# Optimization experiments

Measured on AMD Instinct MI355X. Metric: run time of the kernel, lower is better.

The kernel has to match this reference:

```python
import jax, jax.numpy as jnp
import numpy as np

N, E, IN, HID, HEADS, OUT = 20000, 320000, 64, 32, 8, 128
EPS_SM = 1e-16


def setup_inputs() -> dict:
    key = jax.random.key(0)
    ks = iter(jax.random.split(key, 40))
    def g(shape, scale=0.1):
        return jax.random.normal(next(ks), shape, dtype=jnp.float32) * scale
    inp = {
        "x": jax.random.normal(next(ks), (N, IN), dtype=jnp.float32),
        "edge_index": jax.random.randint(next(ks), (2, E), 0, N, dtype=jnp.int64),
        # layer 0: GATConv(64 -> 32, heads=8, concat) => dim 256
        "W0": g((IN, HEADS * HID)), "b0": jnp.zeros((HEADS * HID,), jnp.float32),
        "as0": g((HEADS, HID)), "ad0": g((HEADS, HID)),
        "lng0": jnp.ones((HEADS * HID,), jnp.float32), "lnb0": jnp.zeros((HEADS * HID,), jnp.float32),
        "rW0": g((IN, HEADS * HID)), "rb0": jnp.zeros((HEADS * HID,), jnp.float32),
        "rw0": jnp.ones((1,), jnp.float32),
        # layer 1: GATConv(256 -> 32, heads=8, concat) => dim 256, residual = Identity
        "W1": g((HEADS * HID, HEADS * HID)), "b1": jnp.zeros((HEADS * HID,), jnp.float32),
        "as1": g((HEADS, HID)), "ad1": g((HEADS, HID)),
        "lng1": jnp.ones((HEADS * HID,), jnp.float32), "lnb1": jnp.zeros((HEADS * HID,), jnp.float32),
        "rw1": jnp.ones((1,), jnp.float32),
        # layer 2: GATConv(256 -> 128, heads=8, concat=False mean) => dim 128
        "W2": g((HEADS * HID, HEADS * OUT)), "b2": jnp.zeros((OUT,), jnp.float32),
        "as2": g((HEADS, OUT)), "ad2": g((HEADS, OUT)),
        "lng2": jnp.ones((OUT,), jnp.float32), "lnb2": jnp.zeros((OUT,), jnp.float32),
        "rW2": g((HEADS * HID, OUT)), "rb2": jnp.zeros((OUT,), jnp.float32),
        "rw2": jnp.ones((1,), jnp.float32),
    }
    return inp


def _gat_conv(x, src, dst, W, b, a_s, a_d, heads, out_c, concat):
    n = x.shape[0]
    h = (x @ W).reshape(n, heads, out_c)            # [N,H,C]
    al_s = jnp.sum(h * a_s, axis=-1)                 # [N,H]
    al_d = jnp.sum(h * a_d, axis=-1)
    e = jax.nn.leaky_relu(al_s[src] + al_d[dst], 0.2)  # [E,H]
    m = jax.ops.segment_max(e, dst, num_segments=n)
    m = jnp.where(jnp.isfinite(m), m, 0.0)
    ex = jnp.exp(e - m[dst])
    denom = jax.ops.segment_sum(ex, dst, num_segments=n)
    alpha = ex / (denom[dst] + EPS_SM)               # [E,H]
    msg = alpha[:, :, None] * h[src]                 # [E,H,C]
    out = jax.ops.segment_sum(msg, dst, num_segments=n)  # [N,H,C]
    if concat:
        return out.reshape(n, heads * out_c) + b
    return out.mean(axis=1) + b


def _layer_norm(x, g, b, eps=1e-5):
    mu = x.mean(-1, keepdims=True)
    var = x.var(-1, keepdims=True)
    return (x - mu) * jax.lax.rsqrt(var + eps) * g + b


def reference(x, edge_index, W0, b0, as0, ad0, lng0, lnb0, rW0, rb0, rw0,
              W1, b1, as1, ad1, lng1, lnb1, rw1,
              W2, b2, as2, ad2, lng2, lnb2, rW2, rb2, rw2):
    ei = edge_index.astype(jnp.int32)
    ar = jnp.arange(N, dtype=jnp.int32)
    src = jnp.concatenate([ei[0], ar])               # add self loops
    dst = jnp.concatenate([ei[1], ar])

    # layer 0 (eval mode: dropout is identity)
    g0 = _gat_conv(x, src, dst, W0, b0, as0, ad0, HEADS, HID, True)
    h = _layer_norm(g0, lng0, lnb0) + jax.nn.sigmoid(rw0) * (x @ rW0 + rb0)
    h = jax.nn.elu(h)

    # layer 1 (residual projection = Identity)
    g1 = _gat_conv(h, src, dst, W1, b1, as1, ad1, HEADS, HID, True)
    h = jax.nn.elu(_layer_norm(g1, lng1, lnb1) + jax.nn.sigmoid(rw1) * h)

    # layer 2 (concat=False -> mean over heads)
    g2 = _gat_conv(h, src, dst, W2, b2, as2, ad2, HEADS, OUT, False)
    out = _layer_norm(g2, lng2, lnb2) + jax.nn.sigmoid(rw2) * (h @ rW2 + rb2)
    return out
```

## Files before the change

### kernel.cpp

```cpp
#include <hip/hip_runtime.h>
#include <cstddef>
#include <cstdint>

#define NN 20000
#define EE 320000
#define ET (EE + NN)
#define CH 64

typedef __attribute__((ext_vector_type(8))) short bf16x8;
typedef __attribute__((ext_vector_type(4))) float f32x4;

__device__ __forceinline__ unsigned short f2bf_rne(float f) {
  unsigned int u = __float_as_uint(f);
  u += 0x7FFF + ((u >> 16) & 1);
  return (unsigned short)(u >> 16);
}

__device__ __forceinline__ float bf2f(unsigned short b) {
  return __uint_as_float(((unsigned int)b) << 16);
}


__global__ __launch_bounds__(256) void zero_i32(int* __restrict__ p, int n) {
  int i = blockIdx.x * 256 + threadIdx.x;
  if (i < n) p[i] = 0;
}

__global__ __launch_bounds__(256) void zero_f32(float* __restrict__ p, int n) {
  int i = blockIdx.x * 256 + threadIdx.x;
  if (i < n) p[i] = 0.f;
}

__global__ __launch_bounds__(256) void cvt_bf16(const float* __restrict__ src,
                                                unsigned short* __restrict__ dst, int n) {
  int i = blockIdx.x * 256 + threadIdx.x;
  if (i < n) dst[i] = f2bf_rne(src[i]);
}

__global__ void tconv(const float* __restrict__ src, unsigned short* __restrict__ dst,
                      int N) {
  int n = blockIdx.x, k = threadIdx.x, K = blockDim.x;
  dst[(size_t)n * K + k] = f2bf_rne(src[(size_t)k * N + n]);
}

__global__ void build_v16(const float* __restrict__ W2, const float* __restrict__ as2,
                          const float* __restrict__ ad2, unsigned short* __restrict__ V16) {
  int r = blockIdx.x, k = threadIdx.x;
  int h = r & 7;
  const float* av = (r < 8) ? (as2 + h * 128) : (ad2 + h * 128);
  const float* wr = W2 + (size_t)k * 1024 + h * 128;
  float v = 0.f;
#pragma unroll 4
  for (int c = 0; c < 128; ++c) v += wr[c] * av[c];
  V16[(size_t)r * 256 + k] = f2bf_rne(v);
}

__global__ void build_wstk(const float* __restrict__ W2, unsigned short* __restrict__ WT) {
  int c = blockIdx.x, k = threadIdx.x;
#pragma unroll
  for (int h = 0; h < 8; ++h)
    WT[(size_t)c * 2048 + h * 256 + k] = f2bf_rne(0.125f * W2[(size_t)k * 1024 + h * 128 + c]);
}


__global__ __launch_bounds__(256) void count_kernel(const int* __restrict__ ei,
                                                    int* __restrict__ deg) {
  int e = blockIdx.x * 256 + threadIdx.x;
  if (e < EE) {
    int d = ei[EE + e];
    if (d >= 0 && d < NN) atomicAdd(&deg[d], 1);
  }
}

__global__ __launch_bounds__(1024) void scan_blk(const int* __restrict__ deg,
    int* __restrict__ offs, int* __restrict__ bsum) {
  __shared__ int s[1024];
  int b = blockIdx.x, tid = threadIdx.x;
  int i = b * 1024 + tid;
  s[tid] = (i < NN) ? (deg[i] + 1) : 0;
  __syncthreads();
  for (int off = 1; off < 1024; off <<= 1) {
    int t = (tid >= off) ? s[tid - off] : 0;
    __syncthreads();
    s[tid] += t;
    __syncthreads();
  }
  if (i < NN) offs[i + 1] = s[tid];
  if (tid == 1023) bsum[b] = s[1023];
}

__global__ void scan_top(int* __restrict__ bsum, int nb) {
  if (threadIdx.x == 0) {
    int run = 0;
    for (int k = 0; k < nb; ++k) { int t = bsum[k]; bsum[k] = run; run += t; }
  }
}

__global__ __launch_bounds__(256) void scan_add(int* __restrict__ offs,
    const int* __restrict__ bsum) {
  int i = blockIdx.x * 256 + threadIdx.x;
  if (i == 0) offs[0] = 0;
  if (i < NN) offs[i + 1] += bsum[i >> 10];
}

__global__ __launch_bounds__(256) void scatter_kernel(const int* __restrict__ ei,
    const int* __restrict__ offs, int* __restrict__ cursor, int* __restrict__ csr) {
  int e = blockIdx.x * 256 + threadIdx.x;
  if (e >= ET) return;
  int s, d;
  if (e < EE) { s = ei[e]; d = ei[EE + e]; }
  else        { s = e - EE; d = s; }
  if (s < 0 || s >= NN || d < 0 || d >= NN) return;
  int pos = atomicAdd(&cursor[d], 1);
  csr[offs[d] + pos] = s;
}


__global__ __launch_bounds__(256) void gemm_mfma(const unsigned short* __restrict__ A,
    const unsigned short* __restrict__ BT, const float* __restrict__ bias,
    float* __restrict__ C, int M, int K, int ldc) {
  int bm = blockIdx.y * 64, bn = blockIdx.x * 64;
  int tid = threadIdx.x;
  int w = tid >> 6, l = tid & 63;
  int wm = bm + w * 16;
  if (wm >= M) return;
  int lane16 = l & 15, q = l >> 4;
  const unsigned short* ap = A + (size_t)(wm + lane16) * K + q * 8;
  const unsigned short* bp = BT + (size_t)(bn + lane16) * K + q * 8;
  f32x4 acc0 = {0.f, 0.f, 0.f, 0.f}, acc1 = acc0, acc2 = acc0, acc3 = acc0;
#pragma unroll 2
  for (int k0 = 0; k0 < K; k0 += 32) {
    bf16x8 a  = *(const bf16x8*)(ap + k0);
    bf16x8 b0 = *(const bf16x8*)(bp + k0);
    bf16x8 b1 = *(const bf16x8*)(bp + (size_t)16 * K + k0);
    bf16x8 b2 = *(const bf16x8*)(bp + (size_t)32 * K + k0);
    bf16x8 b3 = *(const bf16x8*)(bp + (size_t)48 * K + k0);
    acc0 = __builtin_amdgcn_mfma_f32_16x16x32_bf16(a, b0, acc0, 0, 0, 0);
    acc1 = __builtin_amdgcn_mfma_f32_16x16x32_bf16(a, b1, acc1, 0, 0, 0);
    acc2 = __builtin_amdgcn_mfma_f32_16x16x32_bf16(a, b2, acc2, 0, 0, 0);
    acc3 = __builtin_amdgcn_mfma_f32_16x16x32_bf16(a, b3, acc3, 0, 0, 0);
  }
  int row0 = wm + q * 4;
  int c0 = bn + lane16;
  float bi0 = bias ? bias[c0]      : 0.f;
  float bi1 = bias ? bias[c0 + 16] : 0.f;
  float bi2 = bias ? bias[c0 + 32] : 0.f;
  float bi3 = bias ? bias[c0 + 48] : 0.f;
#pragma unroll
  for (int r = 0; r < 4; ++r) {
    float* crow = C + (size_t)(row0 + r) * ldc;
    crow[c0]      = acc0[r] + bi0;
    crow[c0 + 16] = acc1[r] + bi1;
    crow[c0 + 32] = acc2[r] + bi2;
    crow[c0 + 48] = acc3[r] + bi3;
  }
}

__global__ __launch_bounds__(256) void gemm_mfma_bf_al(const unsigned short* __restrict__ A,
    const unsigned short* __restrict__ BT, unsigned short* __restrict__ C,
    const float* __restrict__ as_w, const float* __restrict__ ad_w,
    float* __restrict__ als, float* __restrict__ ald, int M, int K) {
  int bm = blockIdx.y * 64, bn = blockIdx.x * 64;
  int tid = threadIdx.x;
  int w = tid >> 6, l = tid & 63;
  int wm = bm + w * 16;
  if (wm >= M) return;
  int lane16 = l & 15, q = l >> 4;
  const unsigned short* ap = A + (size_t)(wm + lane16) * K + q * 8;
  const unsigned short* bp = BT + (size_t)(bn + lane16) * K + q * 8;
  f32x4 acc0 = {0.f, 0.f, 0.f, 0.f}, acc1 = acc0, acc2 = acc0, acc3 = acc0;
#pragma unroll 2
  for (int k0 = 0; k0 < K; k0 += 32) {
    bf16x8 a  = *(const bf16x8*)(ap + k0);
    bf16x8 b0 = *(const bf16x8*)(bp + k0);
    bf16x8 b1 = *(const bf16x8*)(bp + (size_t)16 * K + k0);
    bf16x8 b2 = *(const bf16x8*)(bp + (size_t)32 * K + k0);
    bf16x8 b3 = *(const bf16x8*)(bp + (size_t)48 * K + k0);
    acc0 = __builtin_amdgcn_mfma_f32_16x16x32_bf16(a, b0, acc0, 0, 0, 0);
    acc1 = __builtin_amdgcn_mfma_f32_16x16x32_bf16(a, b1, acc1, 0, 0, 0);
    acc2 = __builtin_amdgcn_mfma_f32_16x16x32_bf16(a, b2, acc2, 0, 0, 0);
    acc3 = __builtin_amdgcn_mfma_f32_16x16x32_bf16(a, b3, acc3, 0, 0, 0);
  }
  int row0 = wm + q * 4;
  int c0 = bn + lane16;
#pragma unroll
  for (int r = 0; r < 4; ++r) {
    unsigned short* crow = C + (size_t)(row0 + r) * 256;
    crow[c0]      = f2bf_rne(acc0[r]);
    crow[c0 + 16] = f2bf_rne(acc1[r]);
    crow[c0 + 32] = f2bf_rne(acc2[r]);
    crow[c0 + 48] = f2bf_rne(acc3[r]);
  }
  float asA0 = as_w[c0],      asA1 = as_w[c0 + 16];
  float adA0 = ad_w[c0],      adA1 = ad_w[c0 + 16];
  float asB0 = as_w[c0 + 32], asB1 = as_w[c0 + 48];
  float adB0 = ad_w[c0 + 32], adB1 = ad_w[c0 + 48];
  int hA = (bn >> 5), hB = hA + 1;
#pragma unroll
  for (int r = 0; r < 4; ++r) {
    float sA = acc0[r] * asA0 + acc1[r] * asA1;
    float dA = acc0[r] * adA0 + acc1[r] * adA1;
    float sB = acc2[r] * asB0 + acc3[r] * asB1;
    float dB = acc2[r] * adB0 + acc3[r] * adB1;
#pragma unroll
    for (int off = 8; off >= 1; off >>= 1) {
      sA += __shfl_xor(sA, off);
      dA += __shfl_xor(dA, off);
      sB += __shfl_xor(sB, off);
      dB += __shfl_xor(dB, off);
    }
    if (lane16 == 0) {
      int row = row0 + r;
      als[row * 8 + hA] = sA;
      ald[row * 8 + hA] = dA;
      als[row * 8 + hB] = sB;
      ald[row * 8 + hB] = dB;
    }
  }
}

__global__ __launch_bounds__(256) void gemm_al16(const unsigned short* __restrict__ A,
    const unsigned short* __restrict__ V16, float* __restrict__ als,
    float* __restrict__ ald, int M) {
  int bm = blockIdx.x * 64;
  int tid = threadIdx.x;
  int w = tid >> 6, l = tid & 63;
  int wm = bm + w * 16;
  if (wm >= M) return;
  int lane16 = l & 15, q = l >> 4;
  const unsigned short* ap = A + (size_t)(wm + lane16) * 256 + q * 8;
  const unsigned short* bp = V16 + (size_t)lane16 * 256 + q * 8;
  f32x4 acc = {0.f, 0.f, 0.f, 0.f};
#pragma unroll
  for (int k0 = 0; k0 < 256; k0 += 32) {
    bf16x8 a = *(const bf16x8*)(ap + k0);
    bf16x8 b = *(const bf16x8*)(bp + k0);
    acc = __builtin_amdgcn_mfma_f32_16x16x32_bf16(a, b, acc, 0, 0, 0);
  }
  int row0 = wm + q * 4;
  float* dst = (lane16 < 8) ? als : ald;
  int h = lane16 & 7;
#pragma unroll
  for (int r = 0; r < 4; ++r)
    dst[(size_t)(row0 + r) * 8 + h] = acc[r];
}


__global__ __launch_bounds__(256) void gemm_y_tiled(const unsigned short* __restrict__ A,
    const unsigned short* __restrict__ BT, float* __restrict__ P, int M) {
  __shared__ unsigned short sA[64][72];
  __shared__ unsigned short sB[128][72];
  int bm = blockIdx.x * 64, s = blockIdx.y;
  int tid = threadIdx.x;
  int w = tid >> 6, l = tid & 63;
  int lane16 = l & 15, q = l >> 4;
  int soff = s * 512;
  int r = tid >> 3, c = (tid & 7) * 8;
  int rA0 = min(bm + r, M - 1);
  int rA1 = min(bm + r + 32, M - 1);
  f32x4 acc[8] = {};
#pragma unroll 1
  for (int kt = 0; kt < 8; ++kt) {
    int kb = soff + kt * 64 + c;
    *(bf16x8*)&sA[r][c]      = *(const bf16x8*)(A + (size_t)rA0 * 2048 + kb);
    *(bf16x8*)&sA[r + 32][c] = *(const bf16x8*)(A + (size_t)rA1 * 2048 + kb);
#pragma unroll
    for (int rr = 0; rr < 4; ++rr)
      *(bf16x8*)&sB[r + rr * 32][c] = *(const bf16x8*)(BT + (size_t)(r + rr * 32) * 2048 + kb);
    __syncthreads();
#pragma unroll
    for (int kk = 0; kk < 2; ++kk) {
      bf16x8 a = *(const bf16x8*)&sA[w * 16 + lane16][kk * 32 + q * 8];
#pragma unroll
      for (int t = 0; t < 8; ++t) {
        bf16x8 b = *(const bf16x8*)&sB[t * 16 + lane16][kk * 32 + q * 8];
        acc[t] = __builtin_amdgcn_mfma_f32_16x16x32_bf16(a, b, acc[t], 0, 0, 0);
      }
    }
    __syncthreads();
  }
  int row0 = bm + w * 16 + q * 4;
  float* pbase = P + (size_t)s * ((size_t)M * 128);
#pragma unroll
  for (int r2 = 0; r2 < 4; ++r2) {
    if (row0 + r2 < M) {
      float* prow = pbase + (size_t)(row0 + r2) * 128 + lane16;
#pragma unroll
      for (int t = 0; t < 8; ++t) prow[t * 16] = acc[t][r2];
    }
  }
}


__global__ __launch_bounds__(256) void al2(const float* __restrict__ h,
    const float* __restrict__ aw_s, const float* __restrict__ aw_d,
    float* __restrict__ als, float* __restrict__ ald) {
  int n = blockIdx.x, tid = threadIdx.x;
  int j = tid & 127;
  __shared__ float ss[256], sd[256];
  float v = h[(size_t)n * 256 + tid];
  ss[tid] = v * aw_s[tid];
  sd[tid] = v * aw_d[tid];
  __syncthreads();
  for (int off = 64; off > 0; off >>= 1) {
    if (j < off) { ss[tid] += ss[tid + off]; sd[tid] += sd[tid + off]; }
    __syncthreads();
  }
  if (j == 0) {
    int hh = tid >> 7;
    als[n * 2 + hh] = ss[tid];
    ald[n * 2 + hh] = sd[tid];
  }
}


__global__ __launch_bounds__(256) void agg_epi_v2(const unsigned short* __restrict__ hG,
    const float* __restrict__ als, const float* __restrict__ ald,
    const int* __restrict__ offs, const int* __restrict__ csr,
    const float* __restrict__ bias, const float* __restrict__ lng,
    const float* __restrict__ lnb, const float* __restrict__ res,
    const float* __restrict__ rw, float* __restrict__ out,
    unsigned short* __restrict__ outbf) {
  int n = blockIdx.x, tid = threadIdx.x;
  int r0 = offs[n], r1 = offs[n + 1], deg = r1 - r0;
  __shared__ float s_wred[32];
  __shared__ float s_dninv[8], s_ald[8];
  __shared__ int   s_src[CH];
  __shared__ float s_alpha[CH * 8];
  __shared__ float s_part[1024];
  __shared__ float s_w1[4], s_w2[4];

  int w = tid >> 6, l = tid & 63;
  int j = tid >> 3, h8 = tid & 7;
  if (tid < 8) s_ald[tid] = ald[n * 8 + tid];
  float aldn = ald[n * 8 + h8];
  float sm = 0.f;
  for (int i = r0 + j; i < r1; i += 32) {
    float ev = als[csr[i] * 8 + h8] + aldn;
    ev = ev >= 0.f ? ev : 0.2f * ev;
    sm += __expf(ev);
  }
#pragma unroll
  for (int off = 32; off >= 8; off >>= 1) sm += __shfl_xor(sm, off);
  if (l < 8) s_wred[w * 8 + l] = sm;
  __syncthreads();
  if (tid < 8) {
    float t = s_wred[tid] + s_wred[8 + tid] + s_wred[16 + tid] + s_wred[24 + tid];
    s_dninv[tid] = 1.f / (t + 1e-16f);
  }
  __syncthreads();

  int hl = l >> 3;
  f32x4 acc = {0.f, 0.f, 0.f, 0.f};
  for (int c0 = 0; c0 < deg; c0 += CH) {
    int cn = min(CH, deg - c0);
    if (tid < cn) s_src[tid] = csr[r0 + c0 + tid];
    __syncthreads();
    for (int t = tid; t < cn * 8; t += 256) {
      int e = t >> 3, h = t & 7;
      float ev = als[s_src[e] * 8 + h] + s_ald[h];
      ev = ev >= 0.f ? ev : 0.2f * ev;
      s_alpha[t] = __expf(ev) * s_dninv[h];
    }
    __syncthreads();
    int e = w;
    for (; e + 4 < cn; e += 8) {
      int s0 = s_src[e], s1 = s_src[e + 4];
      float a0 = s_alpha[e * 8 + hl], a1 = s_alpha[(e + 4) * 8 + hl];
      uint2 p0 = *(const uint2*)(hG + (size_t)s0 * 256 + l * 4);
      uint2 p1 = *(const uint2*)(hG + (size_t)s1 * 256 + l * 4);
      f32x4 v0 = {__uint_as_float(p0.x << 16), __uint_as_float(p0.x & 0xFFFF0000u),
                  __uint_as_float(p0.y << 16), __uint_as_float(p0.y & 0xFFFF0000u)};
      f32x4 v1 = {__uint_as_float(p1.x << 16), __uint_as_float(p1.x & 0xFFFF0000u),
                  __uint_as_float(p1.y << 16), __uint_as_float(p1.y & 0xFFFF0000u)};
      acc += a0 * v0;
      acc += a1 * v1;
    }
    if (e < cn) {
      int s0 = s_src[e];
      float a0 = s_alpha[e * 8 + hl];
      uint2 p0 = *(const uint2*)(hG + (size_t)s0 * 256 + l * 4);
      f32x4 v0 = {__uint_as_float(p0.x << 16), __uint_as_float(p0.x & 0xFFFF0000u),
                  __uint_as_float(p0.y << 16), __uint_as_float(p0.y & 0xFFFF0000u)};
      acc += a0 * v0;
    }
    __syncthreads();
  }
  ((f32x4*)s_part)[w * 64 + l] = acc;
  __syncthreads();

  float val = s_part[tid] + s_part[256 + tid] + s_part[512 + tid] + s_part[768 + tid]
            + bias[tid];
  float rres = res[(size_t)n * 256 + tid];
  float v1 = val, v2 = val * val;
#pragma unroll
  for (int off = 32; off >= 1; off >>= 1) {
    v1 += __shfl_xor(v1, off);
    v2 += __shfl_xor(v2, off);
  }
  if (l == 0) { s_w1[w] = v1; s_w2[w] = v2; }
  __syncthreads();
  float tot1 = s_w1[0] + s_w1[1] + s_w1[2] + s_w1[3];
  float tot2 = s_w2[0] + s_w2[1] + s_w2[2] + s_w2[3];
  float mu = tot1 * (1.f / 256.f);
  float var = tot2 * (1.f / 256.f) - mu * mu;
  float rs = rsqrtf(var + 1e-5f);
  float sig = 1.f / (1.f + __expf(-rw[0]));
  float lnv = (val - mu) * rs * lng[tid] + lnb[tid];
  float rv = lnv + sig * rres;
  rv = rv > 0.f ? rv : (__expf(rv) - 1.f);
  out[(size_t)n * 256 + tid] = rv;
  outbf[(size_t)n * 256 + tid] = f2bf_rne(rv);
}


__global__ __launch_bounds__(256) void agg_y(const unsigned short* __restrict__ hbf,
    const float* __restrict__ als, const float* __restrict__ ald,
    const int* __restrict__ offs, const int* __restrict__ csr,
    unsigned short* __restrict__ Y) {
  int n = blockIdx.x, tid = threadIdx.x;
  int r0 = offs[n], r1 = offs[n + 1], deg = r1 - r0;
  __shared__ float s_wred[32];
  __shared__ float s_dninv[8], s_ald[8];
  __shared__ int   s_src[CH];
  __shared__ float s_alpha[CH * 8];
  __shared__ float s_y[2][2048];

  int w = tid >> 6, l = tid & 63;
  int j = tid >> 3, h8 = tid & 7;
  if (tid < 8) s_ald[tid] = ald[n * 8 + tid];
  float aldn = ald[n * 8 + h8];
  float sm = 0.f;
  for (int i = r0 + j; i < r1; i += 32) {
    float ev = als[csr[i] * 8 + h8] + aldn;
    ev = ev >= 0.f ? ev : 0.2f * ev;
    sm += __expf(ev);
  }
#pragma unroll
  for (int off = 32; off >= 8; off >>= 1) sm += __shfl_xor(sm, off);
  if (l < 8) s_wred[w * 8 + l] = sm;
  __syncthreads();
  if (tid < 8) {
    float t = s_wred[tid] + s_wred[8 + tid] + s_wred[16 + tid] + s_wred[24 + tid];
    s_dninv[tid] = 1.f / (t + 1e-16f);
  }
  __syncthreads();

  f32x4 accv[8] = {};
  for (int c0 = 0; c0 < deg; c0 += CH) {
    int cn = min(CH, deg - c0);
    if (tid < cn) s_src[tid] = csr[r0 + c0 + tid];
    __syncthreads();
    for (int t = tid; t < cn * 8; t += 256) {
      int e = t >> 3, h = t & 7;
      float ev = als[s_src[e] * 8 + h] + s_ald[h];
      ev = ev >= 0.f ? ev : 0.2f * ev;
      s_alpha[t] = __expf(ev) * s_dninv[h];
    }
    __syncthreads();
    int e = w;
    for (; e + 4 < cn; e += 8) {
      int s0 = s_src[e], s1 = s_src[e + 4];
      f32x4 a00 = *(const f32x4*)&s_alpha[e * 8];
      f32x4 a01 = *(const f32x4*)&s_alpha[e * 8 + 4];
      f32x4 a10 = *(const f32x4*)&s_alpha[(e + 4) * 8];
      f32x4 a11 = *(const f32x4*)&s_alpha[(e + 4) * 8 + 4];
      uint2 p0 = *(const uint2*)(hbf + (size_t)s0 * 256 + l * 4);
      uint2 p1 = *(const uint2*)(hbf + (size_t)s1 * 256 + l * 4);
      f32x4 v0 = {__uint_as_float(p0.x << 16), __uint_as_float(p0.x & 0xFFFF0000u),
                  __uint_as_float(p0.y << 16), __uint_as_float(p0.y & 0xFFFF0000u)};
      f32x4 v1 = {__uint_as_float(p1.x << 16), __uint_as_float(p1.x & 0xFFFF0000u),
                  __uint_as_float(p1.y << 16), __uint_as_float(p1.y & 0xFFFF0000u)};
#pragma unroll
      for (int h = 0; h < 4; ++h) {
        accv[h]     += a00[h] * v0;
        accv[h + 4] += a01[h] * v0;
        accv[h]     += a10[h] * v1;
        accv[h + 4] += a11[h] * v1;
      }
    }
    if (e < cn) {
      int s0 = s_src[e];
      f32x4 a00 = *(const f32x4*)&s_alpha[e * 8];
      f32x4 a01 = *(const f32x4*)&s_alpha[e * 8 + 4];
      uint2 p0 = *(const uint2*)(hbf + (size_t)s0 * 256 + l * 4);
      f32x4 v0 = {__uint_as_float(p0.x << 16), __uint_as_float(p0.x & 0xFFFF0000u),
                  __uint_as_float(p0.y << 16), __uint_as_float(p0.y & 0xFFFF0000u)};
#pragma unroll
      for (int h = 0; h < 4; ++h) {
        accv[h]     += a00[h] * v0;
        accv[h + 4] += a01[h] * v0;
      }
    }
    __syncthreads();
  }

  if (w >= 2) {
    float* dst = s_y[w - 2];
#pragma unroll
    for (int h = 0; h < 8; ++h) ((f32x4*)&dst[h * 256])[l] = accv[h];
  }
  __syncthreads();
  if (w < 2) {
    const float* srcp = s_y[w];
#pragma unroll
    for (int h = 0; h < 8; ++h) accv[h] += ((const f32x4*)&srcp[h * 256])[l];
  }
  __syncthreads();
  if (w == 1) {
#pragma unroll
    for (int h = 0; h < 8; ++h) ((f32x4*)&s_y[0][h * 256])[l] = accv[h];
  }
  __syncthreads();
  if (w == 0) {
    unsigned short* yrow = Y + (size_t)n * 2048;
#pragma unroll
    for (int h = 0; h < 8; ++h) {
      f32x4 t = accv[h] + ((const f32x4*)&s_y[0][h * 256])[l];
      uint2 pk;
      pk.x = (unsigned)f2bf_rne(t.x) | ((unsigned)f2bf_rne(t.y) << 16);
      pk.y = (unsigned)f2bf_rne(t.z) | ((unsigned)f2bf_rne(t.w) << 16);
      *(uint2*)(yrow + h * 256 + l * 4) = pk;
    }
  }
}


__global__ __launch_bounds__(256) void agg2_pair(const float* __restrict__ h2,
    const float* __restrict__ als, const float* __restrict__ ald,
    const int* __restrict__ offs, const int* __restrict__ csr,
    float* __restrict__ acc_out) {
  int n = blockIdx.x, tid = threadIdx.x;
  int r0 = offs[n], r1 = offs[n + 1];
  __shared__ float s_red[256];
  __shared__ float s_dn[2];
  int hh = tid >> 7, j = tid & 127;
  float aldn = ald[n * 2 + hh];
  float sm = 0.f;
  for (int i = r0 + j; i < r1; i += 128) {
    int s = csr[i];
    float ev = als[s * 2 + hh] + aldn;
    ev = ev >= 0.f ? ev : 0.2f * ev;
    sm += __expf(ev);
  }
  s_red[tid] = sm;
  __syncthreads();
  for (int off = 64; off > 0; off >>= 1) {
    if (j < off) s_red[tid] += s_red[tid + off];
    __syncthreads();
  }
  if (j == 0) s_dn[hh] = s_red[tid] + 1e-16f;
  __syncthreads();
  float dinv = 1.f / s_dn[hh];
  float acc = 0.f;
  for (int i = r0; i < r1; ++i) {
    int s = csr[i];
    float ev = als[s * 2 + hh] + aldn;
    ev = ev >= 0.f ? ev : 0.2f * ev;
    float alpha = __expf(ev) * dinv;
    acc += alpha * h2[(size_t)s * 256 + tid];
  }
  s_red[tid] = acc;
  __syncthreads();
  if (tid < 128)
    acc_out[(size_t)n * 128 + tid] += 0.125f * (s_red[tid] + s_red[tid + 128]);
}


__global__ __launch_bounds__(128) void epi_out_res4(const float* __restrict__ P,
    const float* __restrict__ b2, const float* __restrict__ lng,
    const float* __restrict__ lnb, const float* __restrict__ res2,
    const float* __restrict__ rw, float* __restrict__ out) {
  int n = blockIdx.x, tid = threadIdx.x;
  __shared__ float sw1[2], sw2[2];
  size_t stride = (size_t)NN * 128;
  size_t idx = (size_t)n * 128 + tid;
  float g = P[idx] + P[stride + idx] + P[2 * stride + idx] + P[3 * stride + idx] + b2[tid];
  float v1 = g, v2 = g * g;
#pragma unroll
  for (int off = 32; off >= 1; off >>= 1) {
    v1 += __shfl_xor(v1, off);
    v2 += __shfl_xor(v2, off);
  }
  if ((tid & 63) == 0) { sw1[tid >> 6] = v1; sw2[tid >> 6] = v2; }
  __syncthreads();
  float tot1 = sw1[0] + sw1[1], tot2 = sw2[0] + sw2[1];
  float mu = tot1 * (1.f / 128.f);
  float var = tot2 * (1.f / 128.f) - mu * mu;
  float rs = rsqrtf(var + 1e-5f);
  float sig = 1.f / (1.f + __expf(-rw[0]));
  out[idx] = (g - mu) * rs * lng[tid] + lnb[tid] + sig * res2[idx];
}

__global__ __launch_bounds__(128) void epi_out_res(float* __restrict__ acc,
    const float* __restrict__ b2, const float* __restrict__ lng,
    const float* __restrict__ lnb, const float* __restrict__ res2,
    const float* __restrict__ rw) {
  int n = blockIdx.x, tid = threadIdx.x;
  __shared__ float s1[128], s2[128];
  __shared__ float s_mu, s_rs;
  float g = acc[(size_t)n * 128 + tid] + b2[tid];
  s1[tid] = g; s2[tid] = g * g;
  __syncthreads();
  for (int off = 64; off > 0; off >>= 1) {
    if (tid < off) { s1[tid] += s1[tid + off]; s2[tid] += s2[tid + off]; }
    __syncthreads();
  }
  if (tid == 0) {
    float mu = s1[0] * (1.f / 128.f);
    float var = s2[0] * (1.f / 128.f) - mu * mu;
    s_mu = mu; s_rs = rsqrtf(var + 1e-5f);
  }
  __syncthreads();
  float sig = 1.f / (1.f + __expf(-rw[0]));
  float lnv = (g - s_mu) * s_rs * lng[tid] + lnb[tid];
  acc[(size_t)n * 128 + tid] = lnv + sig * res2[(size_t)n * 128 + tid];
}

__global__ __launch_bounds__(128) void epi_out_mv(float* __restrict__ acc,
    const float* __restrict__ b2, const float* __restrict__ lng,
    const float* __restrict__ lnb, const float* __restrict__ hB,
    const float* __restrict__ rW2, const float* __restrict__ rb2,
    const float* __restrict__ rw) {
  int n = blockIdx.x, tid = threadIdx.x;
  __shared__ float srow[256];
  __shared__ float s1[128], s2[128];
  __shared__ float s_mu, s_rs;
  srow[tid] = hB[(size_t)n * 256 + tid];
  srow[tid + 128] = hB[(size_t)n * 256 + tid + 128];
  float g = acc[(size_t)n * 128 + tid] + b2[tid];
  s1[tid] = g; s2[tid] = g * g;
  __syncthreads();
  for (int off = 64; off > 0; off >>= 1) {
    if (tid < off) { s1[tid] += s1[tid + off]; s2[tid] += s2[tid + off]; }
    __syncthreads();
  }
  if (tid == 0) {
    float mu = s1[0] * (1.f / 128.f);
    float var = s2[0] * (1.f / 128.f) - mu * mu;
    s_mu = mu; s_rs = rsqrtf(var + 1e-5f);
  }
  __syncthreads();
  float rv = rb2[tid];
#pragma unroll 4
  for (int k = 0; k < 256; ++k) rv += srow[k] * rW2[(size_t)k * 128 + tid];
  float sig = 1.f / (1.f + __expf(-rw[0]));
  float lnv = (g - s_mu) * s_rs * lng[tid] + lnb[tid];
  acc[(size_t)n * 128 + tid] = lnv + sig * rv;
}


extern "C" void kernel_launch(void* const* d_in, const int* in_sizes, int n_in,
                              void* d_out, int out_size, void* d_ws, size_t ws_size,
                              hipStream_t stream) {
  const float* x   = (const float*)d_in[0];
  const int*   ei  = (const int*)d_in[1];
  const float* W0  = (const float*)d_in[2];
  const float* b0  = (const float*)d_in[3];
  const float* as0 = (const float*)d_in[4];
  const float* ad0 = (const float*)d_in[5];
  const float* lng0= (const float*)d_in[6];
  const float* lnb0= (const float*)d_in[7];
  const float* rW0 = (const float*)d_in[8];
  const float* rb0 = (const float*)d_in[9];
  const float* rw0 = (const float*)d_in[10];
  const float* W1  = (const float*)d_in[11];
  const float* b1  = (const float*)d_in[12];
  const float* as1 = (const float*)d_in[13];
  const float* ad1 = (const float*)d_in[14];
  const float* lng1= (const float*)d_in[15];
  const float* lnb1= (const float*)d_in[16];
  const float* rw1 = (const float*)d_in[17];
  const float* W2  = (const float*)d_in[18];
  const float* b2  = (const float*)d_in[19];
  const float* as2 = (const float*)d_in[20];
  const float* ad2 = (const float*)d_in[21];
  const float* lng2= (const float*)d_in[22];
  const float* lnb2= (const float*)d_in[23];
  const float* rW2 = (const float*)d_in[24];
  const float* rb2 = (const float*)d_in[25];
  const float* rw2 = (const float*)d_in[26];
  float* outp = (float*)d_out;

  char* w = (char*)d_ws;
  auto carve = [&](size_t bytes) -> char* {
    char* p = w;
    w += (bytes + 255) & ~(size_t)255;
    return p;
  };
  float* bufH = (float*)carve((size_t)NN * 256 * 4);
  float* bufR = (float*)carve((size_t)NN * 256 * 4);
  float* als  = (float*)carve((size_t)NN * 8 * 4);
  float* ald  = (float*)carve((size_t)NN * 8 * 4);
  int* deg    = (int*)carve((size_t)2 * NN * 4);
  int* cursor = deg + NN;
  int* offs   = (int*)carve((size_t)(NN + 1) * 4);
  int* bsum   = (int*)carve((size_t)32 * 4);
  int* csr    = (int*)carve((size_t)ET * 4);
  unsigned short* xbf  = (unsigned short*)carve((size_t)NN * 64 * 2);
  unsigned short* hbf  = (unsigned short*)carve((size_t)NN * 256 * 2);
  unsigned short* W0T  = (unsigned short*)carve((size_t)256 * 64 * 2);
  unsigned short* rW0T = (unsigned short*)carve((size_t)256 * 64 * 2);
  unsigned short* W1T  = (unsigned short*)carve((size_t)256 * 256 * 2);
  unsigned short* W2T  = (unsigned short*)carve((size_t)1024 * 256 * 2);
  unsigned short* rW2T = (unsigned short*)carve((size_t)128 * 256 * 2);
  size_t base = (size_t)(w - (char*)d_ws);
  if (ws_size < base) return;
  unsigned short* hG = (unsigned short*)bufH;

  size_t full_extra = (((size_t)16 * 256 * 2 + 255) & ~(size_t)255)
                    + (((size_t)128 * 2048 * 2 + 255) & ~(size_t)255)
                    + (((size_t)NN * 2048 * 2 + 255) & ~(size_t)255);
  size_t res2_extra = (((size_t)NN * 128 * 4 + 255) & ~(size_t)255);
  bool full = (ws_size - base) >= full_extra;
  unsigned short *V16 = nullptr, *WstkT = nullptr, *Ybuf = nullptr;
  if (full) {
    V16   = (unsigned short*)carve((size_t)16 * 256 * 2);
    WstkT = (unsigned short*)carve((size_t)128 * 2048 * 2);
    Ybuf  = (unsigned short*)carve((size_t)NN * 2048 * 2);
  }
  float* res2 = nullptr;
  if ((ws_size - (size_t)(w - (char*)d_ws)) >= res2_extra)
    res2 = (float*)carve((size_t)NN * 128 * 4);

  zero_i32<<<(2 * NN + 255) / 256, 256, 0, stream>>>(deg, 2 * NN);
  count_kernel<<<(EE + 255) / 256, 256, 0, stream>>>(ei, deg);
  int nb = (NN + 1023) / 1024;
  scan_blk<<<nb, 1024, 0, stream>>>(deg, offs, bsum);
  scan_top<<<1, 64, 0, stream>>>(bsum, nb);
  scan_add<<<(NN + 255) / 256, 256, 0, stream>>>(offs, bsum);
  scatter_kernel<<<(ET + 255) / 256, 256, 0, stream>>>(ei, offs, cursor, csr);

  cvt_bf16<<<(NN * 64 + 255) / 256, 256, 0, stream>>>(x, xbf, NN * 64);
  tconv<<<256, 64, 0, stream>>>(W0, W0T, 256);
  tconv<<<256, 64, 0, stream>>>(rW0, rW0T, 256);
  tconv<<<256, 256, 0, stream>>>(W1, W1T, 256);
  tconv<<<128, 256, 0, stream>>>(rW2, rW2T, 128);
  if (full) {
    build_v16<<<16, 256, 0, stream>>>(W2, as2, ad2, V16);
    build_wstk<<<128, 256, 0, stream>>>(W2, WstkT);
  } else {
    tconv<<<1024, 256, 0, stream>>>(W2, W2T, 1024);
  }

  dim3 g256(4, (NN + 63) / 64);
  dim3 g128(2, (NN + 63) / 64);

  gemm_mfma_bf_al<<<g256, 256, 0, stream>>>(xbf, W0T, hG, as0, ad0, als, ald, NN, 64);
  gemm_mfma<<<g256, 256, 0, stream>>>(xbf, rW0T, rb0, bufR, NN, 64, 256);
  agg_epi_v2<<<NN, 256, 0, stream>>>(hG, als, ald, offs, csr, b0, lng0, lnb0,
                                     bufR, rw0, bufR, hbf);

  gemm_mfma_bf_al<<<g256, 256, 0, stream>>>(hbf, W1T, hG, as1, ad1, als, ald, NN, 256);
  agg_epi_v2<<<NN, 256, 0, stream>>>(hG, als, ald, offs, csr, b1, lng1, lnb1,
                                     bufR, rw1, bufR, hbf);

  if (res2)
    gemm_mfma<<<g128, 256, 0, stream>>>(hbf, rW2T, rb2, res2, NN, 256, 128);
  if (full) {
    gemm_al16<<<(NN + 63) / 64, 256, 0, stream>>>(hbf, V16, als, ald, NN);
    agg_y<<<NN, 256, 0, stream>>>(hbf, als, ald, offs, csr, Ybuf);
    if (res2) {
      float* partial = bufH;
      gemm_y_tiled<<<dim3((NN + 63) / 64, 4), 256, 0, stream>>>(Ybuf, WstkT,
                                                                partial, NN);
      epi_out_res4<<<NN, 128, 0, stream>>>(partial, b2, lng2, lnb2, res2, rw2, outp);
    } else {
      gemm_mfma<<<g128, 256, 0, stream>>>(Ybuf, WstkT, nullptr, outp, NN, 2048, 128);
      epi_out_mv<<<NN, 128, 0, stream>>>(outp, b2, lng2, lnb2, bufR, rW2, rb2, rw2);
    }
  } else {
    zero_f32<<<(NN * 128 + 255) / 256, 256, 0, stream>>>(outp, NN * 128);
    for (int p = 0; p < 4; ++p) {
      gemm_mfma<<<g256, 256, 0, stream>>>(hbf, W2T + (size_t)p * 256 * 256, nullptr,
                                          bufH, NN, 256, 256);
      al2<<<NN, 256, 0, stream>>>(bufH, as2 + p * 256, ad2 + p * 256, als, ald);
      agg2_pair<<<NN, 256, 0, stream>>>(bufH, als, ald, offs, csr, outp);
    }
    if (res2)
      epi_out_res<<<NN, 128, 0, stream>>>(outp, b2, lng2, lnb2, res2, rw2);
    else
      epi_out_mv<<<NN, 128, 0, stream>>>(outp, b2, lng2, lnb2, bufR, rW2, rb2, rw2);
  }
}
```

Baseline: 451.4 us.

## Map one wavefront per node in GAT aggregation kernels, single-pass softmax

Rewrites the layer-0/1 aggregation and the layer-2 Y aggregation so each 64-lane wavefront handles one destination node instead of a whole 256-thread block. Source indices and attention exponents are shared through lane shuffles, removing shared memory and block barriers. The separate denominator pass over the edges is folded into the main loop, with normalization applied at the end. The cost is less memory-level parallelism per node, since one wave walks the edges serially, and per-lane register pressure in agg_y_w rises with eight accumulators plus eight denominators.

Result: faster. 423.7 us (-6.1%).

```diff
diff --git a/kernel.cpp b/kernel.cpp
--- a/kernel.cpp
+++ b/kernel.cpp
@@ -5,7 +5,6 @@
 #define NN 20000
 #define EE 320000
 #define ET (EE + NN)
-#define CH 64
 
 typedef __attribute__((ext_vector_type(8))) short bf16x8;
 typedef __attribute__((ext_vector_type(4))) float f32x4;
@@ -314,214 +313,117 @@
 }
 
 
-__global__ __launch_bounds__(256) void agg_epi_v2(const unsigned short* __restrict__ hG,
+__global__ __launch_bounds__(256) void agg_epi_w(const unsigned short* __restrict__ hG,
     const float* __restrict__ als, const float* __restrict__ ald,
     const int* __restrict__ offs, const int* __restrict__ csr,
     const float* __restrict__ bias, const float* __restrict__ lng,
     const float* __restrict__ lnb, const float* __restrict__ res,
     const float* __restrict__ rw, float* __restrict__ out,
     unsigned short* __restrict__ outbf) {
-  int n = blockIdx.x, tid = threadIdx.x;
+  int w = threadIdx.x >> 6, l = threadIdx.x & 63;
+  int n = blockIdx.x * 4 + w;
+  if (n >= NN) return;
   int r0 = offs[n], r1 = offs[n + 1], deg = r1 - r0;
-  __shared__ float s_wred[32];
-  __shared__ float s_dninv[8], s_ald[8];
-  __shared__ int   s_src[CH];
-  __shared__ float s_alpha[CH * 8];
-  __shared__ float s_part[1024];
-  __shared__ float s_w1[4], s_w2[4];
-
-  int w = tid >> 6, l = tid & 63;
-  int j = tid >> 3, h8 = tid & 7;
-  if (tid < 8) s_ald[tid] = ald[n * 8 + tid];
+  int h8 = l & 7;
+  int e8 = l >> 3;
+  int hl = l >> 3;
   float aldn = ald[n * 8 + h8];
-  float sm = 0.f;
-  for (int i = r0 + j; i < r1; i += 32) {
-    float ev = als[csr[i] * 8 + h8] + aldn;
+  f32x4 acc = {0.f, 0.f, 0.f, 0.f};
+  float den = 0.f;
+  for (int c0 = 0; c0 < deg; c0 += 8) {
+    int cn = min(8, deg - c0);
+    int src_my = csr[r0 + c0 + min(e8, cn - 1)];
+    float ev = als[src_my * 8 + h8] + aldn;
     ev = ev >= 0.f ? ev : 0.2f * ev;
-    sm += __expf(ev);
-  }
-#pragma unroll
-  for (int off = 32; off >= 8; off >>= 1) sm += __shfl_xor(sm, off);
-  if (l < 8) s_wred[w * 8 + l] = sm;
-  __syncthreads();
-  if (tid < 8) {
-    float t = s_wred[tid] + s_wred[8 + tid] + s_wred[16 + tid] + s_wred[24 + tid];
-    s_dninv[tid] = 1.f / (t + 1e-16f);
-  }
-  __syncthreads();
-
-  int hl = l >> 3;
-  f32x4 acc = {0.f, 0.f, 0.f, 0.f};
-  for (int c0 = 0; c0 < deg; c0 += CH) {
-    int cn = min(CH, deg - c0);
-    if (tid < cn) s_src[tid] = csr[r0 + c0 + tid];
-    __syncthreads();
-    for (int t = tid; t < cn * 8; t += 256) {
-      int e = t >> 3, h = t & 7;
-      float ev = als[s_src[e] * 8 + h] + s_ald[h];
-      ev = ev >= 0.f ? ev : 0.2f * ev;
-      s_alpha[t] = __expf(ev) * s_dninv[h];
-    }
-    __syncthreads();
-    int e = w;
-    for (; e + 4 < cn; e += 8) {
-      int s0 = s_src[e], s1 = s_src[e + 4];
-      float a0 = s_alpha[e * 8 + hl], a1 = s_alpha[(e + 4) * 8 + hl];
-      uint2 p0 = *(const uint2*)(hG + (size_t)s0 * 256 + l * 4);
-      uint2 p1 = *(const uint2*)(hG + (size_t)s1 * 256 + l * 4);
-      f32x4 v0 = {__uint_as_float(p0.x << 16), __uint_as_float(p0.x & 0xFFFF0000u),
-                  __uint_as_float(p0.y << 16), __uint_as_float(p0.y & 0xFFFF0000u)};
-      f32x4 v1 = {__uint_as_float(p1.x << 16), __uint_as_float(p1.x & 0xFFFF0000u),
-                  __uint_as_float(p1.y << 16), __uint_as_float(p1.y & 0xFFFF0000u)};
-      acc += a0 * v0;
-      acc += a1 * v1;
-    }
-    if (e < cn) {
-      int s0 = s_src[e];
-      float a0 = s_alpha[e * 8 + hl];
-      uint2 p0 = *(const uint2*)(hG + (size_t)s0 * 256 + l * 4);
-      f32x4 v0 = {__uint_as_float(p0.x << 16), __uint_as_float(p0.x & 0xFFFF0000u),
-                  __uint_as_float(p0.y << 16), __uint_as_float(p0.y & 0xFFFF0000u)};
-      acc += a0 * v0;
-    }
-    __syncthreads();
-  }
-  ((f32x4*)s_part)[w * 64 + l] = acc;
-  __syncthreads();
-
-  float val = s_part[tid] + s_part[256 + tid] + s_part[512 + tid] + s_part[768 + tid]
-            + bias[tid];
-  float rres = res[(size_t)n * 256 + tid];
-  float v1 = val, v2 = val * val;
+    float aexp = (e8 < cn) ? __expf(ev) : 0.f;
+#pragma unroll 2
+    for (int e = 0; e < cn; ++e) {
+      int s = __shfl(src_my, e * 8);
+      float a = __shfl(aexp, e * 8 + hl);
+      uint2 p = *(const uint2*)(hG + (size_t)s * 256 + l * 4);
+      f32x4 v = {__uint_as_float(p.x << 16), __uint_as_float(p.x & 0xFFFF0000u),
+                 __uint_as_float(p.y << 16), __uint_as_float(p.y & 0xFFFF0000u)};
+      acc += a * v;
+      den += a;
+    }
+  }
+  float dinv = 1.f / (den + 1e-16f);
+  float4 bi = ((const float4*)bias)[l];
+  float4 rr = ((const float4*)res)[(size_t)n * 64 + l];
+  f32x4 val = {acc.x * dinv + bi.x, acc.y * dinv + bi.y,
+               acc.z * dinv + bi.z, acc.w * dinv + bi.w};
+  float v1 = val.x + val.y + val.z + val.w;
+  float v2 = val.x * val.x + val.y * val.y + val.z * val.z + val.w * val.w;
 #pragma unroll
   for (int off = 32; off >= 1; off >>= 1) {
     v1 += __shfl_xor(v1, off);
     v2 += __shfl_xor(v2, off);
   }
-  if (l == 0) { s_w1[w] = v1; s_w2[w] = v2; }
-  __syncthreads();
-  float tot1 = s_w1[0] + s_w1[1] + s_w1[2] + s_w1[3];
-  float tot2 = s_w2[0] + s_w2[1] + s_w2[2] + s_w2[3];
-  float mu = tot1 * (1.f / 256.f);
-  float var = tot2 * (1.f / 256.f) - mu * mu;
+  float mu = v1 * (1.f / 256.f);
+  float var = v2 * (1.f / 256.f) - mu * mu;
   float rs = rsqrtf(var + 1e-5f);
   float sig = 1.f / (1.f + __expf(-rw[0]));
-  float lnv = (val - mu) * rs * lng[tid] + lnb[tid];
-  float rv = lnv + sig * rres;
-  rv = rv > 0.f ? rv : (__expf(rv) - 1.f);
-  out[(size_t)n * 256 + tid] = rv;
-  outbf[(size_t)n * 256 + tid] = f2bf_rne(rv);
-}
-
-
-__global__ __launch_bounds__(256) void agg_y(const unsigned short* __restrict__ hbf,
+  float4 lg = ((const float4*)lng)[l];
+  float4 lb = ((const float4*)lnb)[l];
+  float4 ov;
+  float* ovp = &ov.x;
+  const float* valp = (const float*)&val;
+  const float* lgp = &lg.x;
+  const float* lbp = &lb.x;
+  const float* rrp = &rr.x;
+#pragma unroll
+  for (int k = 0; k < 4; ++k) {
+    float rv = (valp[k] - mu) * rs * lgp[k] + lbp[k] + sig * rrp[k];
+    ovp[k] = rv > 0.f ? rv : (__expf(rv) - 1.f);
+  }
+  ((float4*)out)[(size_t)n * 64 + l] = ov;
+  uint2 pk;
+  pk.x = (unsigned)f2bf_rne(ov.x) | ((unsigned)f2bf_rne(ov.y) << 16);
+  pk.y = (unsigned)f2bf_rne(ov.z) | ((unsigned)f2bf_rne(ov.w) << 16);
+  ((uint2*)outbf)[(size_t)n * 64 + l] = pk;
+}
+
+
+__global__ __launch_bounds__(256) void agg_y_w(const unsigned short* __restrict__ hbf,
     const float* __restrict__ als, const float* __restrict__ ald,
     const int* __restrict__ offs, const int* __restrict__ csr,
     unsigned short* __restrict__ Y) {
-  int n = blockIdx.x, tid = threadIdx.x;
+  int w = threadIdx.x >> 6, l = threadIdx.x & 63;
+  int n = blockIdx.x * 4 + w;
+  if (n >= NN) return;
   int r0 = offs[n], r1 = offs[n + 1], deg = r1 - r0;
-  __shared__ float s_wred[32];
-  __shared__ float s_dninv[8], s_ald[8];
-  __shared__ int   s_src[CH];
-  __shared__ float s_alpha[CH * 8];
-  __shared__ float s_y[2][2048];
-
-  int w = tid >> 6, l = tid & 63;
-  int j = tid >> 3, h8 = tid & 7;
-  if (tid < 8) s_ald[tid] = ald[n * 8 + tid];
+  int h8 = l & 7, e8 = l >> 3;
   float aldn = ald[n * 8 + h8];
-  float sm = 0.f;
-  for (int i = r0 + j; i < r1; i += 32) {
-    float ev = als[csr[i] * 8 + h8] + aldn;
+  f32x4 accv[8] = {};
+  float den[8] = {};
+  for (int c0 = 0; c0 < deg; c0 += 8) {
+    int cn = min(8, deg - c0);
+    int src_my = csr[r0 + c0 + min(e8, cn - 1)];
+    float ev = als[src_my * 8 + h8] + aldn;
     ev = ev >= 0.f ? ev : 0.2f * ev;
-    sm += __expf(ev);
-  }
-#pragma unroll
-  for (int off = 32; off >= 8; off >>= 1) sm += __shfl_xor(sm, off);
-  if (l < 8) s_wred[w * 8 + l] = sm;
-  __syncthreads();
-  if (tid < 8) {
-    float t = s_wred[tid] + s_wred[8 + tid] + s_wred[16 + tid] + s_wred[24 + tid];
-    s_dninv[tid] = 1.f / (t + 1e-16f);
-  }
-  __syncthreads();
-
-  f32x4 accv[8] = {};
-  for (int c0 = 0; c0 < deg; c0 += CH) {
-    int cn = min(CH, deg - c0);
-    if (tid < cn) s_src[tid] = csr[r0 + c0 + tid];
-    __syncthreads();
-    for (int t = tid; t < cn * 8; t += 256) {
-      int e = t >> 3, h = t & 7;
-      float ev = als[s_src[e] * 8 + h] + s_ald[h];
-      ev = ev >= 0.f ? ev : 0.2f * ev;
-      s_alpha[t] = __expf(ev) * s_dninv[h];
-    }
-    __syncthreads();
-    int e = w;
-    for (; e + 4 < cn; e += 8) {
-      int s0 = s_src[e], s1 = s_src[e + 4];
-      f32x4 a00 = *(const f32x4*)&s_alpha[e * 8];
-      f32x4 a01 = *(const f32x4*)&s_alpha[e * 8 + 4];
-      f32x4 a10 = *(const f32x4*)&s_alpha[(e + 4) * 8];
-      f32x4 a11 = *(const f32x4*)&s_alpha[(e + 4) * 8 + 4];
-      uint2 p0 = *(const uint2*)(hbf + (size_t)s0 * 256 + l * 4);
-      uint2 p1 = *(const uint2*)(hbf + (size_t)s1 * 256 + l * 4);
-      f32x4 v0 = {__uint_as_float(p0.x << 16), __uint_as_float(p0.x & 0xFFFF0000u),
-                  __uint_as_float(p0.y << 16), __uint_as_float(p0.y & 0xFFFF0000u)};
-      f32x4 v1 = {__uint_as_float(p1.x << 16), __uint_as_float(p1.x & 0xFFFF0000u),
-                  __uint_as_float(p1.y << 16), __uint_as_float(p1.y & 0xFFFF0000u)};
-#pragma unroll
-      for (int h = 0; h < 4; ++h) {
-        accv[h]     += a00[h] * v0;
-        accv[h + 4] += a01[h] * v0;
-        accv[h]     += a10[h] * v1;
-        accv[h + 4] += a11[h] * v1;
+    float aexp = (e8 < cn) ? __expf(ev) : 0.f;
+    for (int e = 0; e < cn; ++e) {
+      int s = __shfl(src_my, e * 8);
+      uint2 p = *(const uint2*)(hbf + (size_t)s * 256 + l * 4);
+      f32x4 v = {__uint_as_float(p.x << 16), __uint_as_float(p.x & 0xFFFF0000u),
+                 __uint_as_float(p.y << 16), __uint_as_float(p.y & 0xFFFF0000u)};
+#pragma unroll
+      for (int h = 0; h < 8; ++h) {
+        float a = __shfl(aexp, e * 8 + h);
+        accv[h] += a * v;
+        den[h] += a;
       }
     }
-    if (e < cn) {
-      int s0 = s_src[e];
-      f32x4 a00 = *(const f32x4*)&s_alpha[e * 8];
-      f32x4 a01 = *(const f32x4*)&s_alpha[e * 8 + 4];
-      uint2 p0 = *(const uint2*)(hbf + (size_t)s0 * 256 + l * 4);
-      f32x4 v0 = {__uint_as_float(p0.x << 16), __uint_as_float(p0.x & 0xFFFF0000u),
-                  __uint_as_float(p0.y << 16), __uint_as_float(p0.y & 0xFFFF0000u)};
-#pragma unroll
-      for (int h = 0; h < 4; ++h) {
-        accv[h]     += a00[h] * v0;
-        accv[h + 4] += a01[h] * v0;
-      }
-    }
-    __syncthreads();
-  }
-
-  if (w >= 2) {
-    float* dst = s_y[w - 2];
-#pragma unroll
-    for (int h = 0; h < 8; ++h) ((f32x4*)&dst[h * 256])[l] = accv[h];
-  }
-  __syncthreads();
-  if (w < 2) {
-    const float* srcp = s_y[w];
-#pragma unroll
-    for (int h = 0; h < 8; ++h) accv[h] += ((const f32x4*)&srcp[h * 256])[l];
-  }
-  __syncthreads();
-  if (w == 1) {
-#pragma unroll
-    for (int h = 0; h < 8; ++h) ((f32x4*)&s_y[0][h * 256])[l] = accv[h];
-  }
-  __syncthreads();
-  if (w == 0) {
-    unsigned short* yrow = Y + (size_t)n * 2048;
-#pragma unroll
-    for (int h = 0; h < 8; ++h) {
-      f32x4 t = accv[h] + ((const f32x4*)&s_y[0][h * 256])[l];
-      uint2 pk;
-      pk.x = (unsigned)f2bf_rne(t.x) | ((unsigned)f2bf_rne(t.y) << 16);
-      pk.y = (unsigned)f2bf_rne(t.z) | ((unsigned)f2bf_rne(t.w) << 16);
-      *(uint2*)(yrow + h * 256 + l * 4) = pk;
-    }
+  }
+  unsigned short* yrow = Y + (size_t)n * 2048;
+#pragma unroll
+  for (int h = 0; h < 8; ++h) {
+    float sc = 1.f / (den[h] + 1e-16f);
+    f32x4 t = accv[h];
+    uint2 pk;
+    pk.x = (unsigned)f2bf_rne(t.x * sc) | ((unsigned)f2bf_rne(t.y * sc) << 16);
+    pk.y = (unsigned)f2bf_rne(t.z * sc) | ((unsigned)f2bf_rne(t.w * sc) << 16);
+    *(uint2*)(yrow + h * 256 + l * 4) = pk;
   }
 }
 
@@ -745,21 +647,22 @@
 
   dim3 g256(4, (NN + 63) / 64);
   dim3 g128(2, (NN + 63) / 64);
+  int gagg = (NN + 3) / 4;
 
   gemm_mfma_bf_al<<<g256, 256, 0, stream>>>(xbf, W0T, hG, as0, ad0, als, ald, NN, 64);
   gemm_mfma<<<g256, 256, 0, stream>>>(xbf, rW0T, rb0, bufR, NN, 64, 256);
-  agg_epi_v2<<<NN, 256, 0, stream>>>(hG, als, ald, offs, csr, b0, lng0, lnb0,
-                                     bufR, rw0, bufR, hbf);
+  agg_epi_w<<<gagg, 256, 0, stream>>>(hG, als, ald, offs, csr, b0, lng0, lnb0,
+                                      bufR, rw0, bufR, hbf);
 
   gemm_mfma_bf_al<<<g256, 256, 0, stream>>>(hbf, W1T, hG, as1, ad1, als, ald, NN, 256);
-  agg_epi_v2<<<NN, 256, 0, stream>>>(hG, als, ald, offs, csr, b1, lng1, lnb1,
-                                     bufR, rw1, bufR, hbf);
+  agg_epi_w<<<gagg, 256, 0, stream>>>(hG, als, ald, offs, csr, b1, lng1, lnb1,
+                                      bufR, rw1, bufR, hbf);
 
   if (res2)
     gemm_mfma<<<g128, 256, 0, stream>>>(hbf, rW2T, rb2, res2, NN, 256, 128);
   if (full) {
     gemm_al16<<<(NN + 63) / 64, 256, 0, stream>>>(hbf, V16, als, ald, NN);
-    agg_y<<<NN, 256, 0, stream>>>(hbf, als, ald, offs, csr, Ybuf);
+    agg_y_w<<<gagg, 256, 0, stream>>>(hbf, als, ald, offs, csr, Ybuf);
     if (res2) {
       float* partial = bufH;
       gemm_y_tiled<<<dim3((NN + 63) / 64, 4), 256, 0, stream>>>(Ybuf, WstkT,
```
